# Kernel optimization log

Hardware: AMD Instinct MI355X
Metric: run time of the kernel (lower is better)

The kernel has to match this reference:

```python
import jax, jax.numpy as jnp
import numpy as np

NEG_SLOPE = 0.2


def gat_layer(x, src, dst, W, a_src, a_dst, bias, heads, ch, n):
    # x: [N, F_in]; W: [F_in, heads*ch]; a_src/a_dst: [heads, ch]; bias: [heads*ch]
    h = (x @ W).reshape(n, heads, ch)                      # [N, H, C]
    e_src = (h * a_src[None]).sum(-1)                      # [N, H]
    e_dst = (h * a_dst[None]).sum(-1)                      # [N, H]
    e = jax.nn.leaky_relu(e_src[src] + e_dst[dst], NEG_SLOPE)  # [E, H]
    # segment softmax over incoming edges of each dst node
    m = jax.ops.segment_max(e, dst, num_segments=n)        # [N, H]
    e = jnp.exp(e - m[dst])
    denom = jax.ops.segment_sum(e, dst, num_segments=n)    # [N, H]
    alpha = e / (denom[dst] + 1e-16)                       # [E, H]
    msg = h[src] * alpha[:, :, None]                       # [E, H, C]
    out = jax.ops.segment_sum(msg, dst, num_segments=n)    # [N, H, C]
    return out.reshape(n, heads * ch) + bias


def setup_inputs() -> dict:
    key = jax.random.key(0)
    ks = jax.random.split(key, 12)
    N, E, F_IN, C, H = 50000, 1600000, 128, 64, 4
    x = jax.random.normal(ks[0], (N, F_IN), dtype=jnp.float32)
    edge_index = jax.random.randint(ks[1], (2, E), 0, N, dtype=jnp.int32)
    s = 0.1
    return {
        "x": x,
        "edge_index": edge_index,
        "W1": jax.random.normal(ks[2], (F_IN, H * C), dtype=jnp.float32) * s,
        "a_src1": jax.random.normal(ks[3], (H, C), dtype=jnp.float32) * s,
        "a_dst1": jax.random.normal(ks[4], (H, C), dtype=jnp.float32) * s,
        "b1": jnp.zeros((H * C,), dtype=jnp.float32),
        "W2": jax.random.normal(ks[5], (H * C, C), dtype=jnp.float32) * s,
        "a_src2": jax.random.normal(ks[6], (1, C), dtype=jnp.float32) * s,
        "a_dst2": jax.random.normal(ks[7], (1, C), dtype=jnp.float32) * s,
        "b2": jnp.zeros((C,), dtype=jnp.float32),
        "Wout": jax.random.normal(ks[8], (C, 1), dtype=jnp.float32) * s,
        "bout": jnp.zeros((1,), dtype=jnp.float32),
    }


def reference(x, edge_index, W1, a_src1, a_dst1, b1, W2, a_src2, a_dst2, b2, Wout, bout):
    n = x.shape[0]
    # PyG GATConv default add_self_loops=True
    loop = jnp.arange(n, dtype=edge_index.dtype)
    src = jnp.concatenate([edge_index[0], loop])
    dst = jnp.concatenate([edge_index[1], loop])
    h = gat_layer(x, src, dst, W1, a_src1, a_dst1, b1, heads=4, ch=64, n=n)
    h = jax.nn.relu(h)
    h = gat_layer(h, src, dst, W2, a_src2, a_dst2, b2, heads=1, ch=64, n=n)
    h = jax.nn.relu(h)
    logits = (h @ Wout + bout).squeeze(-1)  # [N]
    return logits
```

## Files before the change

### kernel.cpp

```cpp
#include <hip/hip_runtime.h>
#include <hip/hip_bf16.h>

#define NEG_SLOPE 0.2f

using bf16x8 = __attribute__((ext_vector_type(8))) short;
using f32x4  = __attribute__((ext_vector_type(4))) float;

__device__ __forceinline__ unsigned short f2b(float f) {
  unsigned int u = __float_as_uint(f);
  unsigned int r = (u + 0x7FFFu + ((u >> 16) & 1u)) >> 16;
  return (unsigned short)r;
}
__device__ __forceinline__ float b2f(unsigned short v) {
  return __uint_as_float(((unsigned int)v) << 16);
}
__device__ __forceinline__ float leaky_exp(float e) {
  e = e > 0.f ? e : NEG_SLOPE * e;
  return __expf(e);
}

__global__ void k_prep(const float* __restrict__ W1,
                       const float* __restrict__ W2,
                       const float* __restrict__ a_src1,
                       const float* __restrict__ a_dst1,
                       unsigned short* __restrict__ W1h,
                       unsigned short* __restrict__ W1l,
                       unsigned short* __restrict__ W2h,
                       unsigned short* __restrict__ W2l,
                       float* __restrict__ va,
                       int* __restrict__ ghist) {
  int b = blockIdx.x;
  int t = threadIdx.x;
  if (b < 16) {
    int g = b * 256 + t;
    int l = g & 63, tt = (g >> 6) & 3, kc = (g >> 8) & 3, h = (g >> 10) & 3;
    int n = h * 64 + tt * 16 + (l & 15);
    int kbase = kc * 32 + (l >> 4) * 8;
    size_t base = ((((size_t)h * 4 + kc) * 4 + tt) * 64 + l) * 8;
#pragma unroll
    for (int j = 0; j < 8; j++) {
      float v = W1[(size_t)(kbase + j) * 256 + n];
      unsigned short hi = f2b(v);
      W1h[base + j] = hi;
      W1l[base + j] = f2b(v - b2f(hi));
    }
  } else if (b < 24) {
    int g = (b - 16) * 256 + t;
    int l = g & 63, tt = (g >> 6) & 3, kc = (g >> 8) & 7;
    int n = tt * 16 + (l & 15);
    int kbase = kc * 32 + (l >> 4) * 8;
    size_t base = (((size_t)kc * 4 + tt) * 64 + l) * 8;
#pragma unroll
    for (int j = 0; j < 8; j++) {
      float v = W2[(size_t)(kbase + j) * 64 + n];
      unsigned short hi = f2b(v);
      W2h[base + j] = hi;
      W2l[base + j] = f2b(v - b2f(hi));
    }
  } else if (b < 28) {
    int g = (b - 24) * 256 + t;
    int k = g >> 3, j = g & 7;
    int h = j & 3;
    const float* a = (j < 4) ? a_src1 : a_dst1;
    float s = 0.f;
    for (int c = 0; c < 64; c++) s += W1[(size_t)k * 256 + h * 64 + c] * a[h * 64 + c];
    va[k * 8 + j] = s;
  } else {
    ghist[t] = 0;
  }
}

__global__ __launch_bounds__(256) void k_gh_mfma(const unsigned short* __restrict__ Ab,
                                                 const unsigned short* __restrict__ W1h,
                                                 const unsigned short* __restrict__ W1l,
                                                 const float* __restrict__ b1,
                                                 unsigned short* __restrict__ hact_hi,
                                                 unsigned short* __restrict__ hact_lo,
                                                 int M) {
  const int w = threadIdx.x >> 6, l = threadIdx.x & 63;
  const int h = blockIdx.z;
  const int rowA = blockIdx.x * 64 + w * 16 + (l & 15);
  const int rA = rowA < M ? rowA : M - 1;
  const int kg = l >> 4;
  const unsigned short* Aptr = Ab + (size_t)rA * 512 + h * 128 + kg * 8;
  f32x4 acc[4] = {{0.f, 0.f, 0.f, 0.f}, {0.f, 0.f, 0.f, 0.f},
                  {0.f, 0.f, 0.f, 0.f}, {0.f, 0.f, 0.f, 0.f}};
#pragma unroll
  for (int kc = 0; kc < 4; kc++) {
    bf16x8 a = *reinterpret_cast<const bf16x8*>(Aptr + kc * 32);
#pragma unroll
    for (int t = 0; t < 4; t++) {
      size_t base = ((((size_t)h * 4 + kc) * 4 + t) * 64 + l) * 8;
      bf16x8 bh = *reinterpret_cast<const bf16x8*>(W1h + base);
      bf16x8 bl = *reinterpret_cast<const bf16x8*>(W1l + base);
      acc[t] = __builtin_amdgcn_mfma_f32_16x16x32_bf16(a, bh, acc[t], 0, 0, 0);
      acc[t] = __builtin_amdgcn_mfma_f32_16x16x32_bf16(a, bl, acc[t], 0, 0, 0);
    }
  }
  const int orow0 = blockIdx.x * 64 + w * 16 + (l >> 4) * 4;
  const int col16 = l & 15;
#pragma unroll
  for (int t = 0; t < 4; t++) {
    int col = h * 64 + t * 16 + col16;
    float bb = b1[col];
#pragma unroll
    for (int r = 0; r < 4; r++) {
      int row = orow0 + r;
      if (row < M) {
        float v = fmaxf(acc[t][r] + bb, 0.f);
        unsigned short hi = f2b(v);
        hact_hi[(size_t)row * 256 + col] = hi;
        hact_lo[(size_t)row * 256 + col] = f2b(v - b2f(hi));
      }
    }
  }
}

__global__ __launch_bounds__(256) void k_g2_mfma(const unsigned short* __restrict__ Ahi,
                                                 const unsigned short* __restrict__ Alo,
                                                 const unsigned short* __restrict__ W2h,
                                                 const unsigned short* __restrict__ W2l,
                                                 unsigned short* __restrict__ h2b,
                                                 int M) {
  const int w = threadIdx.x >> 6, l = threadIdx.x & 63;
  const int rowA = blockIdx.x * 64 + w * 16 + (l & 15);
  const int rA = rowA < M ? rowA : M - 1;
  const int kg = l >> 4;
  const unsigned short* Ah = Ahi + (size_t)rA * 256 + kg * 8;
  const unsigned short* Al = Alo + (size_t)rA * 256 + kg * 8;
  f32x4 acc[4] = {{0.f, 0.f, 0.f, 0.f}, {0.f, 0.f, 0.f, 0.f},
                  {0.f, 0.f, 0.f, 0.f}, {0.f, 0.f, 0.f, 0.f}};
#pragma unroll
  for (int kc = 0; kc < 8; kc++) {
    bf16x8 ah = *reinterpret_cast<const bf16x8*>(Ah + kc * 32);
    bf16x8 al = *reinterpret_cast<const bf16x8*>(Al + kc * 32);
#pragma unroll
    for (int t = 0; t < 4; t++) {
      size_t base = (((size_t)kc * 4 + t) * 64 + l) * 8;
      bf16x8 bh = *reinterpret_cast<const bf16x8*>(W2h + base);
      bf16x8 bl = *reinterpret_cast<const bf16x8*>(W2l + base);
      acc[t] = __builtin_amdgcn_mfma_f32_16x16x32_bf16(ah, bh, acc[t], 0, 0, 0);
      acc[t] = __builtin_amdgcn_mfma_f32_16x16x32_bf16(ah, bl, acc[t], 0, 0, 0);
      acc[t] = __builtin_amdgcn_mfma_f32_16x16x32_bf16(al, bh, acc[t], 0, 0, 0);
    }
  }
  const int orow0 = blockIdx.x * 64 + w * 16 + (l >> 4) * 4;
  const int col16 = l & 15;
#pragma unroll
  for (int t = 0; t < 4; t++) {
    int col = t * 16 + col16;
#pragma unroll
    for (int r = 0; r < 4; r++) {
      int row = orow0 + r;
      if (row < M) h2b[(size_t)row * 64 + col] = f2b(acc[t][r]);
    }
  }
}

__global__ __launch_bounds__(256) void k_sxh(const float* __restrict__ x,
                                             const float* __restrict__ va,
                                             float* __restrict__ s_src,
                                             float* __restrict__ s_dst,
                                             unsigned short* __restrict__ xb,
                                             int N, int nsx,
                                             const int* __restrict__ ei,
                                             int E, int Etot,
                                             int* __restrict__ ghist) {
  __shared__ int lh[256];
  if (blockIdx.x >= nsx) {
    int t = threadIdx.x;
    lh[t] = 0;
    __syncthreads();
    int base = ((blockIdx.x - nsx) * 256 + t) * 8;
#pragma unroll
    for (int j = 0; j < 8; j++) {
      int e = base + j;
      if (e < Etot) {
        int dst = (e < E) ? ei[E + e] : (e - E);
        atomicAdd(&lh[dst >> 8], 1);
      }
    }
    __syncthreads();
    if (lh[t]) atomicAdd(&ghist[t], lh[t]);
    return;
  }
  int n = blockIdx.x * 4 + (threadIdx.x >> 6);
  if (n >= N) return;
  int lane = threadIdx.x & 63;
  float x0 = x[(size_t)n * 128 + lane];
  float x1 = x[(size_t)n * 128 + 64 + lane];
  xb[(size_t)n * 128 + lane] = f2b(x0);
  xb[(size_t)n * 128 + 64 + lane] = f2b(x1);
  float4 vs0 = *reinterpret_cast<const float4*>(va + lane * 8);
  float4 vd0 = *reinterpret_cast<const float4*>(va + lane * 8 + 4);
  float4 vs1 = *reinterpret_cast<const float4*>(va + (lane + 64) * 8);
  float4 vd1 = *reinterpret_cast<const float4*>(va + (lane + 64) * 8 + 4);
  float rs0 = x0 * vs0.x + x1 * vs1.x, rs1 = x0 * vs0.y + x1 * vs1.y;
  float rs2 = x0 * vs0.z + x1 * vs1.z, rs3 = x0 * vs0.w + x1 * vs1.w;
  float rd0 = x0 * vd0.x + x1 * vd1.x, rd1 = x0 * vd0.y + x1 * vd1.y;
  float rd2 = x0 * vd0.z + x1 * vd1.z, rd3 = x0 * vd0.w + x1 * vd1.w;
#pragma unroll
  for (int off = 32; off; off >>= 1) {
    rs0 += __shfl_xor(rs0, off, 64); rs1 += __shfl_xor(rs1, off, 64);
    rs2 += __shfl_xor(rs2, off, 64); rs3 += __shfl_xor(rs3, off, 64);
    rd0 += __shfl_xor(rd0, off, 64); rd1 += __shfl_xor(rd1, off, 64);
    rd2 += __shfl_xor(rd2, off, 64); rd3 += __shfl_xor(rd3, off, 64);
  }
  if (lane == 0) {
    float4 ss = {rs0, rs1, rs2, rs3};
    float4 dd = {rd0, rd1, rd2, rd3};
    *reinterpret_cast<float4*>(s_src + (size_t)n * 4) = ss;
    *reinterpret_cast<float4*>(s_dst + (size_t)n * 4) = dd;
  }
}

__global__ __launch_bounds__(256) void k_scores2(const unsigned short* __restrict__ h2b,
                                                 const float* __restrict__ a_src,
                                                 const float* __restrict__ a_dst,
                                                 float* __restrict__ s_src,
                                                 float* __restrict__ s_dst,
                                                 int N) {
  int n = blockIdx.x * 4 + (threadIdx.x >> 6);
  if (n >= N) return;
  int lane = threadIdx.x & 63;
  float hv = b2f(h2b[(size_t)n * 64 + lane]);
  float sv = hv * a_src[lane];
  float dv = hv * a_dst[lane];
#pragma unroll
  for (int off = 32; off; off >>= 1) {
    sv += __shfl_xor(sv, off, 64);
    dv += __shfl_xor(dv, off, 64);
  }
  if (lane == 0) {
    s_src[n] = sv;
    s_dst[n] = dv;
  }
}

__global__ __launch_bounds__(256) void k_scan196(const int* __restrict__ ghist,
                                                 int* __restrict__ bstart,
                                                 int* __restrict__ gcur,
                                                 int nbuck, int Etot) {
  __shared__ int ws[4];
  int t = threadIdx.x;
  int lane = t & 63, wid = t >> 6;
  int v = (t < nbuck) ? ghist[t] : 0;
  int x = v;
#pragma unroll
  for (int off = 1; off < 64; off <<= 1) {
    int y = __shfl_up(x, off, 64);
    if (lane >= off) x += y;
  }
  if (lane == 63) ws[wid] = x;
  __syncthreads();
  if (t == 0) {
    int a0 = ws[0], a1 = ws[1], a2 = ws[2];
    ws[0] = 0; ws[1] = a0; ws[2] = a0 + a1; ws[3] = a0 + a1 + a2;
  }
  __syncthreads();
  int excl = x - v + ws[wid];
  if (t < nbuck) {
    bstart[t] = excl;
    gcur[t] = excl;
  }
  if (t == 0) bstart[nbuck] = Etot;
}

__global__ void k_scatterA(const int* __restrict__ ei, int E, int Etot,
                           int* __restrict__ gcur,
                           int* __restrict__ keys1,
                           int* __restrict__ vals1) {
  __shared__ int lh[256];
  int t = threadIdx.x;
  lh[t] = 0;
  __syncthreads();
  int base = (blockIdx.x * 256 + t) * 8;
  int dsts[8], srcs[8];
#pragma unroll
  for (int j = 0; j < 8; j++) {
    int e = base + j;
    if (e < Etot) {
      int d, s;
      if (e < E) { d = ei[E + e]; s = ei[e]; }
      else       { d = s = e - E; }
      dsts[j] = d; srcs[j] = s;
      atomicAdd(&lh[d >> 8], 1);
    } else dsts[j] = -1;
  }
  __syncthreads();
  {
    int c = lh[t];
    lh[t] = c ? atomicAdd(&gcur[t], c) : 0;
  }
  __syncthreads();
#pragma unroll
  for (int j = 0; j < 8; j++) {
    if (dsts[j] >= 0) {
      int pos = atomicAdd(&lh[dsts[j] >> 8], 1);
      keys1[pos] = dsts[j];
      vals1[pos] = srcs[j];
    }
  }
}

__global__ __launch_bounds__(256) void k_sortB(const int* __restrict__ keys1,
                                               const int* __restrict__ vals1,
                                               const int* __restrict__ bstart,
                                               int* __restrict__ src_sorted,
                                               int* __restrict__ row_ptr,
                                               int N, int Etot) {
  __shared__ int lh[256];
  __shared__ int ws[4];
  int b = blockIdx.x;
  int t = threadIdx.x;
  int lane = t & 63, wid = t >> 6;
  int s = bstart[b], e2 = bstart[b + 1];
  lh[t] = 0;
  __syncthreads();
  for (int p = s + t; p < e2; p += 256)
    atomicAdd(&lh[keys1[p] & 255], 1);
  __syncthreads();
  int v = lh[t];
  int x = v;
#pragma unroll
  for (int off = 1; off < 64; off <<= 1) {
    int y = __shfl_up(x, off, 64);
    if (lane >= off) x += y;
  }
  if (lane == 63) ws[wid] = x;
  __syncthreads();
  if (t == 0) {
    int a0 = ws[0], a1 = ws[1], a2 = ws[2];
    ws[0] = 0; ws[1] = a0; ws[2] = a0 + a1; ws[3] = a0 + a1 + a2;
  }
  __syncthreads();
  int excl = x - v + ws[wid];
  int dst = (b << 8) + t;
  if (dst < N) row_ptr[dst] = s + excl;
  __syncthreads();
  lh[t] = s + excl;
  __syncthreads();
  for (int p = s + t; p < e2; p += 256) {
    int k = keys1[p] & 255;
    int pos = atomicAdd(&lh[k], 1);
    src_sorted[pos] = vals1[p];
  }
  if (b == 0 && t == 0) row_ptr[N] = Etot;
}

__global__ __launch_bounds__(256) void k_w1n(const int* __restrict__ row_ptr,
                                             const int* __restrict__ src_sorted,
                                             const float* __restrict__ s_src,
                                             const float* __restrict__ s_dst,
                                             float4* __restrict__ w1s, int N) {
  int n = blockIdx.x * 4 + (threadIdx.x >> 6);
  if (n >= N) return;
  int lane = threadIdx.x & 63;
  float4 sd = *reinterpret_cast<const float4*>(s_dst + (size_t)n * 4);
  int beg = row_ptr[n], end = row_ptr[n + 1];
  float4 wreg[4];
  float sx = 0.f, sy = 0.f, sz = 0.f, sw = 0.f;
  int i = 0;
  for (int p = beg + lane; p < end; p += 64, i++) {
    int s = src_sorted[p];
    float4 ss = *reinterpret_cast<const float4*>(s_src + (size_t)s * 4);
    float4 w;
    w.x = leaky_exp(ss.x + sd.x);
    w.y = leaky_exp(ss.y + sd.y);
    w.z = leaky_exp(ss.z + sd.z);
    w.w = leaky_exp(ss.w + sd.w);
    if (i < 4) wreg[i] = w; else w1s[p] = w;
    sx += w.x; sy += w.y; sz += w.z; sw += w.w;
  }
#pragma unroll
  for (int off = 32; off; off >>= 1) {
    sx += __shfl_xor(sx, off, 64); sy += __shfl_xor(sy, off, 64);
    sz += __shfl_xor(sz, off, 64); sw += __shfl_xor(sw, off, 64);
  }
  float ix = 1.f / (sx + 1e-16f), iy = 1.f / (sy + 1e-16f);
  float iz = 1.f / (sz + 1e-16f), iw = 1.f / (sw + 1e-16f);
  i = 0;
  for (int p = beg + lane; p < end; p += 64, i++) {
    float4 w = (i < 4) ? wreg[i] : w1s[p];
    w.x *= ix; w.y *= iy; w.z *= iz; w.w *= iw;
    w1s[p] = w;
  }
}

__global__ __launch_bounds__(256) void k_w2n(const int* __restrict__ row_ptr,
                                             const int* __restrict__ src_sorted,
                                             const float* __restrict__ s2s,
                                             const float* __restrict__ s2d,
                                             float* __restrict__ w2s, int N) {
  int n = blockIdx.x * 4 + (threadIdx.x >> 6);
  if (n >= N) return;
  int lane = threadIdx.x & 63;
  float sdn = s2d[n];
  int beg = row_ptr[n], end = row_ptr[n + 1];
  float wreg[4];
  float sum = 0.f;
  int i = 0;
  for (int p = beg + lane; p < end; p += 64, i++) {
    float w = leaky_exp(s2s[src_sorted[p]] + sdn);
    if (i < 4) wreg[i] = w; else w2s[p] = w;
    sum += w;
  }
#pragma unroll
  for (int off = 32; off; off >>= 1) sum += __shfl_xor(sum, off, 64);
  float inv = 1.f / (sum + 1e-16f);
  i = 0;
  for (int p = beg + lane; p < end; p += 64, i++) {
    float w = (i < 4) ? wreg[i] : w2s[p];
    w2s[p] = w * inv;
  }
}

__global__ __launch_bounds__(256) void k_aggx(const unsigned short* __restrict__ xb,
                                              const int* __restrict__ row_ptr,
                                              const int* __restrict__ src_sorted,
                                              const float4* __restrict__ w1s,
                                              unsigned short* __restrict__ avgxb,
                                              int N) {
  int n = blockIdx.x * 4 + (threadIdx.x >> 6);
  if (n >= N) return;
  int lane = threadIdx.x & 63;
  int beg = row_ptr[n], end = row_ptr[n + 1];
  float acc[4][2] = {};
  int p = beg;
  for (; p + 8 <= end; p += 8) {
    int s[8];
    float4 w[8];
    unsigned int pk[8];
#pragma unroll
    for (int j = 0; j < 8; j++) s[j] = src_sorted[p + j];
#pragma unroll
    for (int j = 0; j < 8; j++) w[j] = w1s[p + j];
#pragma unroll
    for (int j = 0; j < 8; j++)
      pk[j] = *reinterpret_cast<const unsigned int*>(xb + (size_t)s[j] * 128 + lane * 2);
#pragma unroll
    for (int j = 0; j < 8; j++) {
      float x0 = __uint_as_float(pk[j] << 16);
      float x1 = __uint_as_float(pk[j] & 0xFFFF0000u);
      acc[0][0] = fmaf(w[j].x, x0, acc[0][0]); acc[0][1] = fmaf(w[j].x, x1, acc[0][1]);
      acc[1][0] = fmaf(w[j].y, x0, acc[1][0]); acc[1][1] = fmaf(w[j].y, x1, acc[1][1]);
      acc[2][0] = fmaf(w[j].z, x0, acc[2][0]); acc[2][1] = fmaf(w[j].z, x1, acc[2][1]);
      acc[3][0] = fmaf(w[j].w, x0, acc[3][0]); acc[3][1] = fmaf(w[j].w, x1, acc[3][1]);
    }
  }
  for (; p < end; p++) {
    int s = src_sorted[p];
    float4 w = w1s[p];
    unsigned int pk = *reinterpret_cast<const unsigned int*>(xb + (size_t)s * 128 + lane * 2);
    float x0 = __uint_as_float(pk << 16);
    float x1 = __uint_as_float(pk & 0xFFFF0000u);
    acc[0][0] = fmaf(w.x, x0, acc[0][0]); acc[0][1] = fmaf(w.x, x1, acc[0][1]);
    acc[1][0] = fmaf(w.y, x0, acc[1][0]); acc[1][1] = fmaf(w.y, x1, acc[1][1]);
    acc[2][0] = fmaf(w.z, x0, acc[2][0]); acc[2][1] = fmaf(w.z, x1, acc[2][1]);
    acc[3][0] = fmaf(w.w, x0, acc[3][0]); acc[3][1] = fmaf(w.w, x1, acc[3][1]);
  }
#pragma unroll
  for (int h = 0; h < 4; h++) {
    unsigned int pk = ((unsigned int)f2b(acc[h][1]) << 16) | f2b(acc[h][0]);
    *reinterpret_cast<unsigned int*>(avgxb + (size_t)n * 512 + h * 128 + lane * 2) = pk;
  }
}

__global__ __launch_bounds__(256) void k_agg2(const unsigned short* __restrict__ h2b,
                                              const int* __restrict__ row_ptr,
                                              const int* __restrict__ src_sorted,
                                              const float* __restrict__ w2s,
                                              const float* __restrict__ bias,
                                              const float* __restrict__ Wout,
                                              const float* __restrict__ bout,
                                              float* __restrict__ logits, int N) {
  int n = blockIdx.x * 4 + (threadIdx.x >> 6);
  if (n >= N) return;
  int lane = threadIdx.x & 63;
  int beg = row_ptr[n], end = row_ptr[n + 1];
  float acc = 0.f;
  int p = beg;
  for (; p + 8 <= end; p += 8) {
    int s[8];
    float w[8];
    unsigned short hv[8];
#pragma unroll
    for (int j = 0; j < 8; j++) s[j] = src_sorted[p + j];
#pragma unroll
    for (int j = 0; j < 8; j++) w[j] = w2s[p + j];
#pragma unroll
    for (int j = 0; j < 8; j++) hv[j] = h2b[(size_t)s[j] * 64 + lane];
#pragma unroll
    for (int j = 0; j < 8; j++) acc = fmaf(w[j], b2f(hv[j]), acc);
  }
  for (; p < end; p++)
    acc = fmaf(w2s[p], b2f(h2b[(size_t)src_sorted[p] * 64 + lane]), acc);
  float o = fmaxf(acc + bias[lane], 0.f);
  float v = o * Wout[lane];
#pragma unroll
  for (int off = 32; off; off >>= 1) v += __shfl_xor(v, off, 64);
  if (lane == 0) logits[n] = v + bout[0];
}

extern "C" void kernel_launch(void* const* d_in, const int* in_sizes, int n_in,
                              void* d_out, int out_size, void* d_ws, size_t ws_size,
                              hipStream_t stream) {
  const float* x      = (const float*)d_in[0];
  const int*   ei     = (const int*)d_in[1];
  const float* W1     = (const float*)d_in[2];
  const float* a_src1 = (const float*)d_in[3];
  const float* a_dst1 = (const float*)d_in[4];
  const float* b1     = (const float*)d_in[5];
  const float* W2     = (const float*)d_in[6];
  const float* a_src2 = (const float*)d_in[7];
  const float* a_dst2 = (const float*)d_in[8];
  const float* b2     = (const float*)d_in[9];
  const float* Wout   = (const float*)d_in[10];
  const float* bout   = (const float*)d_in[11];
  float* logits = (float*)d_out;

  const int HC1  = in_sizes[5];
  const int F_IN = in_sizes[2] / HC1;
  const int N    = in_sizes[0] / F_IN;
  const int E    = in_sizes[1] / 2;
  const int Etot = E + N;
  const int NBUCK = (N + 255) >> 8;

  char* w = (char*)d_ws;
  auto alloc = [&](size_t bytes) {
    char* p = w;
    w += (bytes + 255) & ~(size_t)255;
    return p;
  };
  char* regA = alloc((size_t)N * 128 * sizeof(unsigned short));
  unsigned short* xb = (unsigned short*)regA;
  char* regB = alloc((size_t)N * 512 * sizeof(unsigned short));
  unsigned short* avgxb = (unsigned short*)regB;
  unsigned short* h2b = (unsigned short*)regB;
  float* w2s = (float*)(regB + (size_t)N * 256 * sizeof(unsigned short));
  char* regC = alloc((size_t)N * 256 * 4);
  int* keys1 = (int*)regC;
  int* vals1 = (int*)(regC + (size_t)Etot * 4 + 256);
  float4* w1s = (float4*)regC;
  unsigned short* hact_hi = (unsigned short*)regC;
  unsigned short* hact_lo = (unsigned short*)(regC + (size_t)N * 256 * sizeof(unsigned short));
  float* s_src1  = (float*)alloc((size_t)N * 4 * 4);
  float* s_dst1  = (float*)alloc((size_t)N * 4 * 4);
  float* s2_src  = (float*)alloc((size_t)N * 4);
  float* s2_dst  = (float*)alloc((size_t)N * 4);
  float* va      = (float*)alloc(128 * 8 * 4);
  unsigned short* W1h = (unsigned short*)alloc(4096 * 8 * 2);
  unsigned short* W1l = (unsigned short*)alloc(4096 * 8 * 2);
  unsigned short* W2h = (unsigned short*)alloc(2048 * 8 * 2);
  unsigned short* W2l = (unsigned short*)alloc(2048 * 8 * 2);
  int* row_ptr   = (int*)alloc((size_t)(N + 1) * 4);
  int* src_sorted= (int*)alloc((size_t)Etot * 4);
  int* ghist     = (int*)alloc(256 * 4);
  int* bstart    = (int*)alloc(260 * 4);
  int* gcur      = (int*)alloc(256 * 4);

  k_prep<<<29, 256, 0, stream>>>(W1, W2, a_src1, a_dst1, W1h, W1l, W2h, W2l,
                                 va, ghist);

  const int nsx = (N + 3) / 4;
  const int gsort = (Etot + 2047) / 2048;
  k_sxh<<<nsx + gsort, 256, 0, stream>>>(x, va, s_src1, s_dst1, xb, N, nsx,
                                         ei, E, Etot, ghist);

  k_scan196<<<1, 256, 0, stream>>>(ghist, bstart, gcur, NBUCK, Etot);
  k_scatterA<<<gsort, 256, 0, stream>>>(ei, E, Etot, gcur, keys1, vals1);
  k_sortB<<<NBUCK, 256, 0, stream>>>(keys1, vals1, bstart, src_sorted, row_ptr, N, Etot);

  k_w1n<<<(N + 3) / 4, 256, 0, stream>>>(row_ptr, src_sorted, s_src1, s_dst1, w1s, N);
  k_aggx<<<(N + 3) / 4, 256, 0, stream>>>(xb, row_ptr, src_sorted, w1s, avgxb, N);
  dim3 gh((N + 63) / 64, 1, 4);
  k_gh_mfma<<<gh, 256, 0, stream>>>(avgxb, W1h, W1l, b1, hact_hi, hact_lo, N);

  k_g2_mfma<<<(N + 63) / 64, 256, 0, stream>>>(hact_hi, hact_lo, W2h, W2l, h2b, N);
  k_scores2<<<(N + 3) / 4, 256, 0, stream>>>(h2b, a_src2, a_dst2, s2_src, s2_dst, N);
  k_w2n<<<(N + 3) / 4, 256, 0, stream>>>(row_ptr, src_sorted, s2_src, s2_dst, w2s, N);
  k_agg2<<<(N + 3) / 4, 256, 0, stream>>>(h2b, row_ptr, src_sorted, w2s,
                                          b2, Wout, bout, logits, N);
}
```

Measured before the change: 420.0 us.

## Fuse attention-weight normalization into neighbor aggregation kernels for both layers

Merges the separate softmax-weight kernels (k_w1n, k_w2n) into the aggregation kernels. Each wavefront computes unnormalized edge weights for a chunk of 64 edges, stages the source indices and weights in LDS, accumulates the weighted neighbor features, and divides by the reduced sum at the end. This removes the per-edge weight arrays written to and read back from global memory, plus two kernel launches. In exchange it adds LDS staging and relies on wavefront-local ordering (an lgkmcnt wait rather than a barrier) to make the LDS writes visible.

```diff
diff --git a/kernel.cpp b/kernel.cpp
--- a/kernel.cpp
+++ b/kernel.cpp
@@ -348,154 +348,139 @@
   if (b == 0 && t == 0) row_ptr[N] = Etot;
 }
 
-__global__ __launch_bounds__(256) void k_w1n(const int* __restrict__ row_ptr,
-                                             const int* __restrict__ src_sorted,
-                                             const float* __restrict__ s_src,
-                                             const float* __restrict__ s_dst,
-                                             float4* __restrict__ w1s, int N) {
-  int n = blockIdx.x * 4 + (threadIdx.x >> 6);
+__global__ __launch_bounds__(256) void k_agg1f(const unsigned short* __restrict__ xb,
+                                               const int* __restrict__ row_ptr,
+                                               const int* __restrict__ src_sorted,
+                                               const float* __restrict__ s_src,
+                                               const float* __restrict__ s_dst,
+                                               unsigned short* __restrict__ avgxb,
+                                               int N) {
+  __shared__ int    lsrc[4][64];
+  __shared__ __align__(16) float4 lw[4][64];
+  const int wv = threadIdx.x >> 6;
+  const int n = blockIdx.x * 4 + wv;
   if (n >= N) return;
-  int lane = threadIdx.x & 63;
+  const int lane = threadIdx.x & 63;
   float4 sd = *reinterpret_cast<const float4*>(s_dst + (size_t)n * 4);
   int beg = row_ptr[n], end = row_ptr[n + 1];
-  float4 wreg[4];
-  float sx = 0.f, sy = 0.f, sz = 0.f, sw = 0.f;
-  int i = 0;
-  for (int p = beg + lane; p < end; p += 64, i++) {
-    int s = src_sorted[p];
-    float4 ss = *reinterpret_cast<const float4*>(s_src + (size_t)s * 4);
-    float4 w;
-    w.x = leaky_exp(ss.x + sd.x);
-    w.y = leaky_exp(ss.y + sd.y);
-    w.z = leaky_exp(ss.z + sd.z);
-    w.w = leaky_exp(ss.w + sd.w);
-    if (i < 4) wreg[i] = w; else w1s[p] = w;
-    sx += w.x; sy += w.y; sz += w.z; sw += w.w;
+  float acc[4][2] = {};
+  float ws0 = 0.f, ws1 = 0.f, ws2 = 0.f, ws3 = 0.f;
+
+  for (int base = beg; base < end; base += 64) {
+    int cnt = end - base;
+    if (cnt > 64) cnt = 64;
+    if (lane < cnt) {
+      int s = src_sorted[base + lane];
+      float4 ss = *reinterpret_cast<const float4*>(s_src + (size_t)s * 4);
+      float4 w;
+      w.x = leaky_exp(ss.x + sd.x);
+      w.y = leaky_exp(ss.y + sd.y);
+      w.z = leaky_exp(ss.z + sd.z);
+      w.w = leaky_exp(ss.w + sd.w);
+      lsrc[wv][lane] = s;
+      lw[wv][lane] = w;
+      ws0 += w.x; ws1 += w.y; ws2 += w.z; ws3 += w.w;
+    }
+    __asm__ volatile("s_waitcnt lgkmcnt(0)" ::: "memory");
+    int j = 0;
+    for (; j + 8 <= cnt; j += 8) {
+      int s[8];
+      float4 w[8];
+      unsigned int pk[8];
+#pragma unroll
+      for (int q = 0; q < 8; q++) s[q] = lsrc[wv][j + q];
+#pragma unroll
+      for (int q = 0; q < 8; q++) w[q] = lw[wv][j + q];
+#pragma unroll
+      for (int q = 0; q < 8; q++)
+        pk[q] = *reinterpret_cast<const unsigned int*>(xb + (size_t)s[q] * 128 + lane * 2);
+#pragma unroll
+      for (int q = 0; q < 8; q++) {
+        float x0 = __uint_as_float(pk[q] << 16);
+        float x1 = __uint_as_float(pk[q] & 0xFFFF0000u);
+        acc[0][0] = fmaf(w[q].x, x0, acc[0][0]); acc[0][1] = fmaf(w[q].x, x1, acc[0][1]);
+        acc[1][0] = fmaf(w[q].y, x0, acc[1][0]); acc[1][1] = fmaf(w[q].y, x1, acc[1][1]);
+        acc[2][0] = fmaf(w[q].z, x0, acc[2][0]); acc[2][1] = fmaf(w[q].z, x1, acc[2][1]);
+        acc[3][0] = fmaf(w[q].w, x0, acc[3][0]); acc[3][1] = fmaf(w[q].w, x1, acc[3][1]);
+      }
+    }
+    for (; j < cnt; j++) {
+      int s = lsrc[wv][j];
+      float4 w = lw[wv][j];
+      unsigned int pk = *reinterpret_cast<const unsigned int*>(xb + (size_t)s * 128 + lane * 2);
+      float x0 = __uint_as_float(pk << 16);
+      float x1 = __uint_as_float(pk & 0xFFFF0000u);
+      acc[0][0] = fmaf(w.x, x0, acc[0][0]); acc[0][1] = fmaf(w.x, x1, acc[0][1]);
+      acc[1][0] = fmaf(w.y, x0, acc[1][0]); acc[1][1] = fmaf(w.y, x1, acc[1][1]);
+      acc[2][0] = fmaf(w.z, x0, acc[2][0]); acc[2][1] = fmaf(w.z, x1, acc[2][1]);
+      acc[3][0] = fmaf(w.w, x0, acc[3][0]); acc[3][1] = fmaf(w.w, x1, acc[3][1]);
+    }
   }
 #pragma unroll
   for (int off = 32; off; off >>= 1) {
-    sx += __shfl_xor(sx, off, 64); sy += __shfl_xor(sy, off, 64);
-    sz += __shfl_xor(sz, off, 64); sw += __shfl_xor(sw, off, 64);
-  }
-  float ix = 1.f / (sx + 1e-16f), iy = 1.f / (sy + 1e-16f);
-  float iz = 1.f / (sz + 1e-16f), iw = 1.f / (sw + 1e-16f);
-  i = 0;
-  for (int p = beg + lane; p < end; p += 64, i++) {
-    float4 w = (i < 4) ? wreg[i] : w1s[p];
-    w.x *= ix; w.y *= iy; w.z *= iz; w.w *= iw;
-    w1s[p] = w;
-  }
-}
-
-__global__ __launch_bounds__(256) void k_w2n(const int* __restrict__ row_ptr,
-                                             const int* __restrict__ src_sorted,
-                                             const float* __restrict__ s2s,
-                                             const float* __restrict__ s2d,
-                                             float* __restrict__ w2s, int N) {
-  int n = blockIdx.x * 4 + (threadIdx.x >> 6);
+    ws0 += __shfl_xor(ws0, off, 64); ws1 += __shfl_xor(ws1, off, 64);
+    ws2 += __shfl_xor(ws2, off, 64); ws3 += __shfl_xor(ws3, off, 64);
+  }
+  float inv[4] = {1.f / (ws0 + 1e-16f), 1.f / (ws1 + 1e-16f),
+                  1.f / (ws2 + 1e-16f), 1.f / (ws3 + 1e-16f)};
+#pragma unroll
+  for (int h = 0; h < 4; h++) {
+    unsigned int pk = ((unsigned int)f2b(acc[h][1] * inv[h]) << 16) | f2b(acc[h][0] * inv[h]);
+    *reinterpret_cast<unsigned int*>(avgxb + (size_t)n * 512 + h * 128 + lane * 2) = pk;
+  }
+}
+
+__global__ __launch_bounds__(256) void k_agg2f(const unsigned short* __restrict__ h2b,
+                                               const int* __restrict__ row_ptr,
+                                               const int* __restrict__ src_sorted,
+                                               const float* __restrict__ s2s,
+                                               const float* __restrict__ s2d,
+                                               const float* __restrict__ bias,
+                                               const float* __restrict__ Wout,
+                                               const float* __restrict__ bout,
+                                               float* __restrict__ logits, int N) {
+  __shared__ int   lsrc[4][64];
+  __shared__ float lw[4][64];
+  const int wv = threadIdx.x >> 6;
+  const int n = blockIdx.x * 4 + wv;
   if (n >= N) return;
-  int lane = threadIdx.x & 63;
+  const int lane = threadIdx.x & 63;
   float sdn = s2d[n];
   int beg = row_ptr[n], end = row_ptr[n + 1];
-  float wreg[4];
-  float sum = 0.f;
-  int i = 0;
-  for (int p = beg + lane; p < end; p += 64, i++) {
-    float w = leaky_exp(s2s[src_sorted[p]] + sdn);
-    if (i < 4) wreg[i] = w; else w2s[p] = w;
-    sum += w;
-  }
-#pragma unroll
-  for (int off = 32; off; off >>= 1) sum += __shfl_xor(sum, off, 64);
-  float inv = 1.f / (sum + 1e-16f);
-  i = 0;
-  for (int p = beg + lane; p < end; p += 64, i++) {
-    float w = (i < 4) ? wreg[i] : w2s[p];
-    w2s[p] = w * inv;
-  }
-}
-
-__global__ __launch_bounds__(256) void k_aggx(const unsigned short* __restrict__ xb,
-                                              const int* __restrict__ row_ptr,
-                                              const int* __restrict__ src_sorted,
-                                              const float4* __restrict__ w1s,
-                                              unsigned short* __restrict__ avgxb,
-                                              int N) {
-  int n = blockIdx.x * 4 + (threadIdx.x >> 6);
-  if (n >= N) return;
-  int lane = threadIdx.x & 63;
-  int beg = row_ptr[n], end = row_ptr[n + 1];
-  float acc[4][2] = {};
-  int p = beg;
-  for (; p + 8 <= end; p += 8) {
-    int s[8];
-    float4 w[8];
-    unsigned int pk[8];
-#pragma unroll
-    for (int j = 0; j < 8; j++) s[j] = src_sorted[p + j];
-#pragma unroll
-    for (int j = 0; j < 8; j++) w[j] = w1s[p + j];
-#pragma unroll
-    for (int j = 0; j < 8; j++)
-      pk[j] = *reinterpret_cast<const unsigned int*>(xb + (size_t)s[j] * 128 + lane * 2);
-#pragma unroll
-    for (int j = 0; j < 8; j++) {
-      float x0 = __uint_as_float(pk[j] << 16);
-      float x1 = __uint_as_float(pk[j] & 0xFFFF0000u);
-      acc[0][0] = fmaf(w[j].x, x0, acc[0][0]); acc[0][1] = fmaf(w[j].x, x1, acc[0][1]);
-      acc[1][0] = fmaf(w[j].y, x0, acc[1][0]); acc[1][1] = fmaf(w[j].y, x1, acc[1][1]);
-      acc[2][0] = fmaf(w[j].z, x0, acc[2][0]); acc[2][1] = fmaf(w[j].z, x1, acc[2][1]);
-      acc[3][0] = fmaf(w[j].w, x0, acc[3][0]); acc[3][1] = fmaf(w[j].w, x1, acc[3][1]);
-    }
-  }
-  for (; p < end; p++) {
-    int s = src_sorted[p];
-    float4 w = w1s[p];
-    unsigned int pk = *reinterpret_cast<const unsigned int*>(xb + (size_t)s * 128 + lane * 2);
-    float x0 = __uint_as_float(pk << 16);
-    float x1 = __uint_as_float(pk & 0xFFFF0000u);
-    acc[0][0] = fmaf(w.x, x0, acc[0][0]); acc[0][1] = fmaf(w.x, x1, acc[0][1]);
-    acc[1][0] = fmaf(w.y, x0, acc[1][0]); acc[1][1] = fmaf(w.y, x1, acc[1][1]);
-    acc[2][0] = fmaf(w.z, x0, acc[2][0]); acc[2][1] = fmaf(w.z, x1, acc[2][1]);
-    acc[3][0] = fmaf(w.w, x0, acc[3][0]); acc[3][1] = fmaf(w.w, x1, acc[3][1]);
-  }
-#pragma unroll
-  for (int h = 0; h < 4; h++) {
-    unsigned int pk = ((unsigned int)f2b(acc[h][1]) << 16) | f2b(acc[h][0]);
-    *reinterpret_cast<unsigned int*>(avgxb + (size_t)n * 512 + h * 128 + lane * 2) = pk;
-  }
-}
-
-__global__ __launch_bounds__(256) void k_agg2(const unsigned short* __restrict__ h2b,
-                                              const int* __restrict__ row_ptr,
-                                              const int* __restrict__ src_sorted,
-                                              const float* __restrict__ w2s,
-                                              const float* __restrict__ bias,
-                                              const float* __restrict__ Wout,
-                                              const float* __restrict__ bout,
-                                              float* __restrict__ logits, int N) {
-  int n = blockIdx.x * 4 + (threadIdx.x >> 6);
-  if (n >= N) return;
-  int lane = threadIdx.x & 63;
-  int beg = row_ptr[n], end = row_ptr[n + 1];
-  float acc = 0.f;
-  int p = beg;
-  for (; p + 8 <= end; p += 8) {
-    int s[8];
-    float w[8];
-    unsigned short hv[8];
-#pragma unroll
-    for (int j = 0; j < 8; j++) s[j] = src_sorted[p + j];
-#pragma unroll
-    for (int j = 0; j < 8; j++) w[j] = w2s[p + j];
-#pragma unroll
-    for (int j = 0; j < 8; j++) hv[j] = h2b[(size_t)s[j] * 64 + lane];
-#pragma unroll
-    for (int j = 0; j < 8; j++) acc = fmaf(w[j], b2f(hv[j]), acc);
-  }
-  for (; p < end; p++)
-    acc = fmaf(w2s[p], b2f(h2b[(size_t)src_sorted[p] * 64 + lane]), acc);
-  float o = fmaxf(acc + bias[lane], 0.f);
+  float acc = 0.f, wsp = 0.f;
+
+  for (int base = beg; base < end; base += 64) {
+    int cnt = end - base;
+    if (cnt > 64) cnt = 64;
+    if (lane < cnt) {
+      int s = src_sorted[base + lane];
+      float w = leaky_exp(s2s[s] + sdn);
+      lsrc[wv][lane] = s;
+      lw[wv][lane] = w;
+      wsp += w;
+    }
+    __asm__ volatile("s_waitcnt lgkmcnt(0)" ::: "memory");
+    int j = 0;
+    for (; j + 8 <= cnt; j += 8) {
+      int s[8];
+      float w[8];
+      unsigned short hv[8];
+#pragma unroll
+      for (int q = 0; q < 8; q++) s[q] = lsrc[wv][j + q];
+#pragma unroll
+      for (int q = 0; q < 8; q++) w[q] = lw[wv][j + q];
+#pragma unroll
+      for (int q = 0; q < 8; q++) hv[q] = h2b[(size_t)s[q] * 64 + lane];
+#pragma unroll
+      for (int q = 0; q < 8; q++) acc = fmaf(w[q], b2f(hv[q]), acc);
+    }
+    for (; j < cnt; j++) {
+      acc = fmaf(lw[wv][j], b2f(h2b[(size_t)lsrc[wv][j] * 64 + lane]), acc);
+    }
+  }
+#pragma unroll
+  for (int off = 32; off; off >>= 1) wsp += __shfl_xor(wsp, off, 64);
+  float o = fmaxf(acc / (wsp + 1e-16f) + bias[lane], 0.f);
   float v = o * Wout[lane];
 #pragma unroll
   for (int off = 32; off; off >>= 1) v += __shfl_xor(v, off, 64);
@@ -537,11 +522,9 @@
   char* regB = alloc((size_t)N * 512 * sizeof(unsigned short));
   unsigned short* avgxb = (unsigned short*)regB;
   unsigned short* h2b = (unsigned short*)regB;
-  float* w2s = (float*)(regB + (size_t)N * 256 * sizeof(unsigned short));
   char* regC = alloc((size_t)N * 256 * 4);
   int* keys1 = (int*)regC;
   int* vals1 = (int*)(regC + (size_t)Etot * 4 + 256);
-  float4* w1s = (float4*)regC;
   unsigned short* hact_hi = (unsigned short*)regC;
   unsigned short* hact_lo = (unsigned short*)(regC + (size_t)N * 256 * sizeof(unsigned short));
   float* s_src1  = (float*)alloc((size_t)N * 4 * 4);
@@ -571,14 +554,14 @@
   k_scatterA<<<gsort, 256, 0, stream>>>(ei, E, Etot, gcur, keys1, vals1);
   k_sortB<<<NBUCK, 256, 0, stream>>>(keys1, vals1, bstart, src_sorted, row_ptr, N, Etot);
 
-  k_w1n<<<(N + 3) / 4, 256, 0, stream>>>(row_ptr, src_sorted, s_src1, s_dst1, w1s, N);
-  k_aggx<<<(N + 3) / 4, 256, 0, stream>>>(xb, row_ptr, src_sorted, w1s, avgxb, N);
+  k_agg1f<<<(N + 3) / 4, 256, 0, stream>>>(xb, row_ptr, src_sorted,
+                                           s_src1, s_dst1, avgxb, N);
   dim3 gh((N + 63) / 64, 1, 4);
   k_gh_mfma<<<gh, 256, 0, stream>>>(avgxb, W1h, W1l, b1, hact_hi, hact_lo, N);
 
   k_g2_mfma<<<(N + 63) / 64, 256, 0, stream>>>(hact_hi, hact_lo, W2h, W2l, h2b, N);
   k_scores2<<<(N + 3) / 4, 256, 0, stream>>>(h2b, a_src2, a_dst2, s2_src, s2_dst, N);
-  k_w2n<<<(N + 3) / 4, 256, 0, stream>>>(row_ptr, src_sorted, s2_src, s2_dst, w2s, N);
-  k_agg2<<<(N + 3) / 4, 256, 0, stream>>>(h2b, row_ptr, src_sorted, w2s,
-                                          b2, Wout, bout, logits, N);
-}
+  k_agg2f<<<(N + 3) / 4, 256, 0, stream>>>(h2b, row_ptr, src_sorted,
+                                           s2_src, s2_dst, b2, Wout, bout,
+                                           logits, N);
+}
```

Result: faster. 372.6 us (-11.3%).
